# Kernel optimization log

Measured on AMD Instinct MI355X. Metric: run time of the kernel, lower is better.

## Reference

```python
import jax, jax.numpy as jnp
import numpy as np
import math

NUM_EMBED = 1024
EMBED_FEATS = 256
IN_FEATS = 512
COMMITMENT_COST = 0.25
B, T = 16, 4096


def setup_inputs() -> dict:
    key = jax.random.key(0)
    k1, k2, k3, k4 = jax.random.split(key, 4)
    inputs = jax.random.normal(k1, (B, IN_FEATS, T), dtype=jnp.float32)
    # Conv1d(kernel_size=1) == per-position linear: weight [E, C_in], bias [E]
    proj_w = jax.random.normal(k2, (EMBED_FEATS, IN_FEATS), dtype=jnp.float32) / np.sqrt(IN_FEATS)
    proj_b = jax.random.normal(k3, (EMBED_FEATS,), dtype=jnp.float32) * 0.01
    embed = jax.random.normal(k4, (NUM_EMBED, EMBED_FEATS), dtype=jnp.float32)
    return {"inputs": inputs, "proj_w": proj_w, "proj_b": proj_b, "embed": embed}


def reference(inputs, proj_w, proj_b, embed):
    sg = jax.lax.stop_gradient
    b, c_in, t = inputs.shape
    # 1x1 conv projection then transpose(1,-1): [B, T, E]
    x = jnp.einsum('bct,ec->bte', inputs, proj_w) + proj_b
    flat = x.reshape(-1, EMBED_FEATS)  # [B*T, E]
    d2 = (jnp.sum(flat * flat, axis=1, keepdims=True)
          + jnp.sum(embed * embed, axis=1)
          - 2.0 * flat @ embed.T)  # [B*T, num_embed]
    q_idx = jnp.argmin(d2, axis=1)  # [B*T]
    # one-hot @ embed == direct gather (same math, same gradient structure)
    z_q = embed[q_idx].reshape(x.shape)  # [B, T, E]
    vq_loss = jnp.mean((z_q - sg(x)) ** 2)
    commitment_loss = jnp.mean((sg(z_q) - x) ** 2)
    loss = vq_loss + COMMITMENT_COST * commitment_loss
    z_q_st = x + sg(z_q - x)  # straight-through
    n_tokens = flat.shape[0]
    probs = jnp.zeros((NUM_EMBED,), dtype=jnp.float32).at[q_idx].add(1.0) / n_tokens
    log_perplexity = -jnp.sum(probs * jnp.log(probs + 1e-10))
    num_spatial = n_tokens / b
    kldiv_r = math.log(NUM_EMBED) * num_spatial * jnp.ones((b, 1), dtype=jnp.float32)
    z_q_out = jnp.swapaxes(z_q_st, 1, 2)  # [B, E, T]
    return z_q_out, loss, kldiv_r, log_perplexity
```

## Files before the change

### kernel.cpp

```cpp
#include <hip/hip_runtime.h>
#include <hip/hip_bf16.h>
#include <math.h>

#define TT   4096
#define BB   16
#define NTOK 65536
#define CIN  512
#define EF   256
#define NE   1024

typedef __attribute__((ext_vector_type(8))) short bf16x8;
typedef __attribute__((ext_vector_type(4))) float f32x4;

static __device__ __forceinline__ unsigned short f2bf(float f) {
  unsigned int u = __float_as_uint(f);
  u += 0x7fffu + ((u >> 16) & 1u);
  return (unsigned short)(u >> 16);
}

#define GLL(gsrc, ldst) \
  __builtin_amdgcn_global_load_lds((const __attribute__((address_space(1))) void*)(gsrc), \
                                   (__attribute__((address_space(3))) void*)(ldst), 16, 0, 0)

__global__ __launch_bounds__(256) void k_prep(const float* __restrict__ Wf,
                                              const float* __restrict__ Ef,
                                              unsigned short* __restrict__ Wbf,
                                              unsigned short* __restrict__ Ebf,
                                              float* __restrict__ e_norm) {
  int bid = blockIdx.x;
  if (bid < 512) {
    int i = bid * 256 + threadIdx.x;
    Wbf[i] = f2bf(Wf[i]);
  } else if (bid < 1536) {
    int i = (bid - 512) * 256 + threadIdx.x;
    Ebf[i] = f2bf(-2.0f * Ef[i]);
  } else {
    int w = threadIdx.x >> 6, l = threadIdx.x & 63;
    int k = (bid - 1536) * 4 + w;
    const float4 v4 = ((const float4*)(Ef + (size_t)k * EF))[l];
    float s = v4.x * v4.x + v4.y * v4.y + v4.z * v4.z + v4.w * v4.w;
    for (int off = 32; off; off >>= 1) s += __shfl_down(s, off);
    if (l == 0) e_norm[k] = s;
  }
}

__global__ __launch_bounds__(512, 2) void k_fused(const float* __restrict__ in,
                                                  const unsigned short* __restrict__ Wbf,
                                                  const float* __restrict__ bias,
                                                  const unsigned short* __restrict__ Ebf,
                                                  const float* __restrict__ e_norm,
                                                  const float* __restrict__ embed,
                                                  unsigned int* __restrict__ hist,
                                                  float* __restrict__ sse,
                                                  float* __restrict__ out) {
  __shared__ unsigned short lds[36864];
  unsigned short* abuf = lds;
  unsigned short* xs = lds;

  int tid = threadIdx.x;
  int w = tid >> 6, l = tid & 63;
  int l15 = l & 15, quad = l >> 4;
  int tq = w & 1, eq = w >> 1;
  int cg = w & 3, th = w >> 2;
  int tok0 = blockIdx.x * 128;
  const float* src = in + (size_t)(tok0 >> 12) * CIN * TT + (tok0 & 4095);

  f32x4 acc[4][4];
#pragma unroll
  for (int a = 0; a < 4; ++a)
#pragma unroll
    for (int b = 0; b < 4; ++b) acc[a][b] = (f32x4){0.f, 0.f, 0.f, 0.f};

  float v0[16], v1[16];
  {
    const float* sA = src + (size_t)(cg * 16) * TT + th * 64 + l;
#pragma unroll
    for (int i = 0; i < 16; ++i) v0[i] = __builtin_nontemporal_load(&sA[(size_t)i * TT]);
    __builtin_amdgcn_sched_barrier(0);
#pragma unroll
    for (int i = 0; i < 4; ++i) {
      int g = i * 512 + tid;
      int row = g >> 3, pc = g & 7, lc = pc ^ (row & 7);
      GLL(Wbf + (size_t)row * CIN + lc * 8, lds + 4096 + g * 8);
    }
    __builtin_amdgcn_sched_barrier(0);
    const float* sB = src + (size_t)(64 + cg * 16) * TT + th * 64 + l;
#pragma unroll
    for (int i = 0; i < 16; ++i) v1[i] = __builtin_nontemporal_load(&sB[(size_t)i * TT]);
    __builtin_amdgcn_sched_barrier(0);
  }
  int trow = th * 64 + l;
#pragma unroll
  for (int ks = 0; ks < 8; ++ks) {
    unsigned short* wb = lds + 4096 + (ks & 1) * 16384;
    const float* vc = (ks & 1) ? v1 : v0;
#pragma unroll
    for (int cc = 0; cc < 2; ++cc) {
      alignas(16) unsigned short tmp[8];
#pragma unroll
      for (int j = 0; j < 8; ++j) tmp[j] = f2bf(vc[cc * 8 + j]);
      int c8 = cg * 2 + cc;
      int pc2 = c8 ^ (trow & 7);
      *(bf16x8*)(abuf + trow * 64 + pc2 * 8) = *(const bf16x8*)tmp;
    }
    if (ks < 7) {
#pragma unroll
      for (int i = 0; i < 4; ++i) {
        int g = i * 512 + tid;
        int row = g >> 3, pc = g & 7, lc = pc ^ (row & 7);
        GLL(Wbf + (size_t)row * CIN + (ks + 1) * 64 + lc * 8,
            lds + 4096 + ((ks + 1) & 1) * 16384 + g * 8);
      }
    }
    __builtin_amdgcn_sched_barrier(0);
    if (ks < 6) {
      float* vn = (ks & 1) ? v1 : v0;
      const float* sN = src + (size_t)((ks + 2) * 64 + cg * 16) * TT + th * 64 + l;
#pragma unroll
      for (int i = 0; i < 16; ++i) vn[i] = __builtin_nontemporal_load(&sN[(size_t)i * TT]);
    }
    __builtin_amdgcn_sched_barrier(0);
    if (ks < 6)       asm volatile("s_waitcnt vmcnt(36) lgkmcnt(0)\n\ts_barrier" ::: "memory");
    else if (ks == 6) asm volatile("s_waitcnt vmcnt(20) lgkmcnt(0)\n\ts_barrier" ::: "memory");
    else              asm volatile("s_waitcnt vmcnt(0) lgkmcnt(0)\n\ts_barrier" ::: "memory");
#pragma unroll
    for (int kstep = 0; kstep < 2; ++kstep) {
      int ck = kstep * 4 + quad;
      bf16x8 af4[4], bfr[4];
#pragma unroll
      for (int msub = 0; msub < 4; ++msub) {
        int row = tq * 64 + msub * 16 + l15;
        int pa = ck ^ (row & 7);
        af4[msub] = *(const bf16x8*)(abuf + row * 64 + pa * 8);
      }
#pragma unroll
      for (int nsub = 0; nsub < 4; ++nsub) {
        int row = eq * 64 + nsub * 16 + l15;
        int pb = ck ^ (row & 7);
        bfr[nsub] = *(const bf16x8*)(wb + row * 64 + pb * 8);
      }
      __builtin_amdgcn_s_setprio(1);
#pragma unroll
      for (int msub = 0; msub < 4; ++msub)
#pragma unroll
        for (int nsub = 0; nsub < 4; ++nsub)
          acc[msub][nsub] = __builtin_amdgcn_mfma_f32_16x16x32_bf16(af4[msub], bfr[nsub],
                                                                    acc[msub][nsub], 0, 0, 0);
      __builtin_amdgcn_s_setprio(0);
    }
    asm volatile("s_waitcnt lgkmcnt(0)\n\ts_barrier" ::: "memory");
  }

  float xsq = 0.f;
#pragma unroll
  for (int nsub = 0; nsub < 4; ++nsub) {
    int e = eq * 64 + nsub * 16 + l15;
    float bv = bias[e];
    int cx = e >> 3;
#pragma unroll
    for (int msub = 0; msub < 4; ++msub)
#pragma unroll
      for (int reg = 0; reg < 4; ++reg) {
        int m = tq * 64 + msub * 16 + quad * 4 + reg;
        float x = acc[msub][nsub][reg] + bv;
        xsq += x * x;
        int pcx = cx ^ (m & 31);
        xs[m * 256 + pcx * 8 + (e & 7)] = f2bf(x);
      }
  }
  __syncthreads();

  int g3 = w & 3, h = w >> 2;
  bf16x8 af[2][8];
#pragma unroll
  for (int msub = 0; msub < 2; ++msub)
#pragma unroll
    for (int kst = 0; kst < 8; ++kst) {
      int row = g3 * 32 + msub * 16 + l15;
      int c32 = kst * 4 + quad;
      int pcx = c32 ^ (row & 31);
      af[msub][kst] = *(const bf16x8*)(xs + row * 256 + pcx * 8);
    }
  __syncthreads();

  float* entab = (float*)(lds + 32768);
  {
    float2 ev = *(const float2*)(e_norm + (tid << 1));
    *(float2*)(entab + (tid << 1)) = ev;
  }
  __builtin_amdgcn_sched_barrier(0);
#pragma unroll
  for (int c = 0; c < 3; ++c)
#pragma unroll
    for (int i = 0; i < 2; ++i) {
      int g = i * 512 + tid;
      int row = g >> 5, pcc = g & 31, lc = pcc ^ row;
      GLL(Ebf + (size_t)(c * 32 + row) * EF + lc * 8, lds + c * 8192 + g * 8);
    }
  __builtin_amdgcn_sched_barrier(0);

  float best_v[2][4];
  int best_i[2][4];
#pragma unroll
  for (int a = 0; a < 2; ++a)
#pragma unroll
    for (int b = 0; b < 4; ++b) { best_v[a][b] = 3.0e38f; best_i[a][b] = 0; }

  int r3 = h * 16 + l15;
#pragma unroll 1
  for (int chunk = 0; chunk < 32; ++chunk) {
    unsigned short* eb = lds + (chunk & 3) * 8192;
    int c0 = chunk * 32;
    if (chunk < 29) {
      unsigned short* ebn = lds + ((chunk + 3) & 3) * 8192;
#pragma unroll
      for (int i = 0; i < 2; ++i) {
        int g = i * 512 + tid;
        int row = g >> 5, pcc = g & 31, lc = pcc ^ row;
        GLL(Ebf + (size_t)(c0 + 96 + row) * EF + lc * 8, ebn + g * 8);
      }
      __builtin_amdgcn_sched_barrier(0);
      asm volatile("s_waitcnt vmcnt(6) lgkmcnt(0)\n\ts_barrier" ::: "memory");
    } else {
      asm volatile("s_waitcnt vmcnt(0) lgkmcnt(0)\n\ts_barrier" ::: "memory");
    }
    float en = entab[c0 + r3];
    f32x4 dacc[2];
    dacc[0] = (f32x4){en, en, en, en};
    dacc[1] = dacc[0];
    __builtin_amdgcn_s_setprio(1);
#pragma unroll
    for (int kst = 0; kst < 8; ++kst) {
      int cc = kst * 4 + quad;
      int pc = cc ^ r3;
      bf16x8 bfr = *(const bf16x8*)(eb + r3 * 256 + pc * 8);
      dacc[0] = __builtin_amdgcn_mfma_f32_16x16x32_bf16(af[0][kst], bfr, dacc[0], 0, 0, 0);
      dacc[1] = __builtin_amdgcn_mfma_f32_16x16x32_bf16(af[1][kst], bfr, dacc[1], 0, 0, 0);
    }
    __builtin_amdgcn_s_setprio(0);
    int code = c0 + r3;
#pragma unroll
    for (int msub = 0; msub < 2; ++msub)
#pragma unroll
      for (int reg = 0; reg < 4; ++reg) {
        float vv = dacc[msub][reg];
        if (vv < best_v[msub][reg]) { best_v[msub][reg] = vv; best_i[msub][reg] = code; }
      }
    asm volatile("s_waitcnt lgkmcnt(0)\n\ts_barrier" ::: "memory");
  }

#pragma unroll
  for (int msub = 0; msub < 2; ++msub)
#pragma unroll
    for (int reg = 0; reg < 4; ++reg) {
      float vv = best_v[msub][reg];
      int idx = best_i[msub][reg];
#pragma unroll
      for (int off = 8; off; off >>= 1) {
        float ov = __shfl_xor(vv, off, 16);
        int oi = __shfl_xor(idx, off, 16);
        if (ov < vv || (ov == vv && oi < idx)) { vv = ov; idx = oi; }
      }
      best_v[msub][reg] = vv;
      best_i[msub][reg] = idx;
    }
  float* red_v = (float*)lds;
  int* red_i = (int*)lds + 256;
  float* xred = (float*)lds + 512;
  float* svred = (float*)lds + 520;
  int* fidx_w = (int*)lds + 544;
  if (l15 == 0) {
#pragma unroll
    for (int msub = 0; msub < 2; ++msub)
#pragma unroll
      for (int reg = 0; reg < 4; ++reg) {
        int tokloc = g3 * 32 + msub * 16 + quad * 4 + reg;
        red_v[h * 128 + tokloc] = best_v[msub][reg];
        red_i[h * 128 + tokloc] = best_i[msub][reg];
      }
  }
  for (int off = 32; off; off >>= 1) xsq += __shfl_down(xsq, off);
  if (l == 0) xred[w] = xsq;
  __syncthreads();
  if (tid < 128) {
    float v0r = red_v[tid], v1r = red_v[128 + tid];
    int i0 = red_i[tid], i1 = red_i[128 + tid];
    float vv; int idx;
    if (v1r < v0r || (v1r == v0r && i1 < i0)) { vv = v1r; idx = i1; } else { vv = v0r; idx = i0; }
    fidx_w[tid] = idx;
    atomicAdd(&hist[idx], 1u);
    for (int off = 32; off; off >>= 1) vv += __shfl_down(vv, off);
    if ((tid & 63) == 0) svred[tid >> 6] = vv;
  }
  __syncthreads();
  if (tid == 0) {
    float tot = svred[0] + svred[1];
#pragma unroll
    for (int i = 0; i < 8; ++i) tot += xred[i];
    atomicAdd(sse, tot);
  }

  const int* fidx = (const int*)lds + 544;
  float* zq = (float*)lds + 1024;
  int bnum = tok0 >> 12, t0 = tok0 & 4095;
  float* outb = out + (((size_t)bnum * EF) << 12) + t0;
#pragma unroll 1
  for (int et = 0; et < 4; ++et) {
    int e0 = et * 64;
#pragma unroll
    for (int rr = 0; rr < 4; ++rr) {
      int tl = rr * 32 + (tid >> 4);
      const float4 g4 = *(const float4*)(embed + (size_t)fidx[tl] * EF + e0 + (tid & 15) * 4);
      float* zr = zq + tl * 65 + (tid & 15) * 4;
      zr[0] = g4.x; zr[1] = g4.y; zr[2] = g4.z; zr[3] = g4.w;
    }
    __syncthreads();
#pragma unroll
    for (int rr = 0; rr < 4; ++rr) {
      int e = rr * 16 + (tid >> 5);
      float* orow = outb + ((size_t)(e0 + e) << 12);
#pragma unroll
      for (int j = 0; j < 4; ++j) {
        int t = (tid & 31) + 32 * j;
        __builtin_nontemporal_store(zq[t * 65 + e], &orow[t]);
      }
    }
    if (et < 3) __syncthreads();
  }
}

__global__ __launch_bounds__(256) void k_final(const unsigned int* __restrict__ hist,
                                               const float* __restrict__ sse,
                                               float* __restrict__ out) {
  __shared__ float red[4];
  int tid = threadIdx.x;
  float local = 0.f;
  for (int i = tid; i < NE; i += 256) {
    float p = (float)hist[i] * (1.0f / 65536.0f);
    local -= p * logf(p + 1e-10f);
  }
  for (int off = 32; off; off >>= 1) local += __shfl_down(local, off);
  if ((tid & 63) == 0) red[tid >> 6] = local;
  __syncthreads();
  if (tid == 0) {
    float lp = red[0] + red[1] + red[2] + red[3];
    out[16777216] = 1.25f * sse[0] / 16777216.0f;
    out[16777233] = lp;
  }
  if (tid < 16) out[16777217 + tid] = 6.93147180559945f * 4096.0f;
}

extern "C" void kernel_launch(void* const* d_in, const int* in_sizes, int n_in,
                              void* d_out, int out_size, void* d_ws, size_t ws_size,
                              hipStream_t stream) {
  const float* inputs = (const float*)d_in[0];
  const float* proj_w = (const float*)d_in[1];
  const float* proj_b = (const float*)d_in[2];
  const float* embed = (const float*)d_in[3];
  float* out = (float*)d_out;
  char* ws = (char*)d_ws;

  unsigned short* Wbf  = (unsigned short*)(ws);
  unsigned short* Ebf  = (unsigned short*)(ws + 262144);
  float* e_norm        = (float*)(ws + 786432);
  unsigned int* hist   = (unsigned int*)(ws + 1052672);
  float* sse           = (float*)(ws + 1056768);
  if (ws_size < 1056772) return;

  hipMemsetAsync(ws + 1052672, 0, 4100, stream);

  k_prep<<<1792, 256, 0, stream>>>(proj_w, embed, Wbf, Ebf, e_norm);
  k_fused<<<512, 512, 0, stream>>>(inputs, Wbf, proj_b, Ebf, e_norm, embed, hist, sse, out);
  k_final<<<1, 256, 0, stream>>>(hist, sse, out);
}
```

Measured before the change: 293.5 us.

## Fold final reduction into fused kernel and drop per-chunk codebook barrier

Replaces the memset and the separate single-block finalize kernel with zeroing inside the prep kernel and a last-block-done atomic counter in the fused kernel, which computes perplexity and loss in-kernel. This removes two launches. The codebook chunk loop now uses one waitcnt plus barrier per iteration, issued before the next prefetch, instead of two barriers. The weight staging region in LDS is moved to a larger offset so it no longer overlaps the area used for other buffers. The risks are extra LDS use per block, which could lower occupancy, and the added complexity of ordering the atomic completion counter correctly.

```diff
diff --git a/kernel.cpp b/kernel.cpp
--- a/kernel.cpp
+++ b/kernel.cpp
@@ -26,7 +26,10 @@
                                               const float* __restrict__ Ef,
                                               unsigned short* __restrict__ Wbf,
                                               unsigned short* __restrict__ Ebf,
-                                              float* __restrict__ e_norm) {
+                                              float* __restrict__ e_norm,
+                                              unsigned int* __restrict__ hist,
+                                              float* __restrict__ sse,
+                                              unsigned int* __restrict__ cnt) {
   int bid = blockIdx.x;
   if (bid < 512) {
     int i = bid * 256 + threadIdx.x;
@@ -34,13 +37,17 @@
   } else if (bid < 1536) {
     int i = (bid - 512) * 256 + threadIdx.x;
     Ebf[i] = f2bf(-2.0f * Ef[i]);
-  } else {
+  } else if (bid < 1792) {
     int w = threadIdx.x >> 6, l = threadIdx.x & 63;
     int k = (bid - 1536) * 4 + w;
     const float4 v4 = ((const float4*)(Ef + (size_t)k * EF))[l];
     float s = v4.x * v4.x + v4.y * v4.y + v4.z * v4.z + v4.w * v4.w;
     for (int off = 32; off; off >>= 1) s += __shfl_down(s, off);
     if (l == 0) e_norm[k] = s;
+  } else {
+    int tid = threadIdx.x;
+    *(uint4*)(hist + tid * 4) = (uint4){0u, 0u, 0u, 0u};
+    if (tid == 0) { *sse = 0.f; *cnt = 0u; }
   }
 }
 
@@ -52,8 +59,9 @@
                                                   const float* __restrict__ embed,
                                                   unsigned int* __restrict__ hist,
                                                   float* __restrict__ sse,
+                                                  unsigned int* __restrict__ cnt,
                                                   float* __restrict__ out) {
-  __shared__ unsigned short lds[36864];
+  __shared__ unsigned short lds[40960];
   unsigned short* abuf = lds;
   unsigned short* xs = lds;
 
@@ -81,7 +89,7 @@
     for (int i = 0; i < 4; ++i) {
       int g = i * 512 + tid;
       int row = g >> 3, pc = g & 7, lc = pc ^ (row & 7);
-      GLL(Wbf + (size_t)row * CIN + lc * 8, lds + 4096 + g * 8);
+      GLL(Wbf + (size_t)row * CIN + lc * 8, lds + 8192 + g * 8);
     }
     __builtin_amdgcn_sched_barrier(0);
     const float* sB = src + (size_t)(64 + cg * 16) * TT + th * 64 + l;
@@ -92,7 +100,7 @@
   int trow = th * 64 + l;
 #pragma unroll
   for (int ks = 0; ks < 8; ++ks) {
-    unsigned short* wb = lds + 4096 + (ks & 1) * 16384;
+    unsigned short* wb = lds + 8192 + (ks & 1) * 16384;
     const float* vc = (ks & 1) ? v1 : v0;
 #pragma unroll
     for (int cc = 0; cc < 2; ++cc) {
@@ -109,7 +117,7 @@
         int g = i * 512 + tid;
         int row = g >> 3, pc = g & 7, lc = pc ^ (row & 7);
         GLL(Wbf + (size_t)row * CIN + (ks + 1) * 64 + lc * 8,
-            lds + 4096 + ((ks + 1) & 1) * 16384 + g * 8);
+            lds + 8192 + ((ks + 1) & 1) * 16384 + g * 8);
       }
     }
     __builtin_amdgcn_sched_barrier(0);
@@ -211,7 +219,10 @@
   for (int chunk = 0; chunk < 32; ++chunk) {
     unsigned short* eb = lds + (chunk & 3) * 8192;
     int c0 = chunk * 32;
-    if (chunk < 29) {
+    if (chunk < 30)       asm volatile("s_waitcnt vmcnt(4) lgkmcnt(0)\n\ts_barrier" ::: "memory");
+    else if (chunk == 30) asm volatile("s_waitcnt vmcnt(2) lgkmcnt(0)\n\ts_barrier" ::: "memory");
+    else                  asm volatile("s_waitcnt vmcnt(0) lgkmcnt(0)\n\ts_barrier" ::: "memory");
+    if (chunk <= 28) {
       unsigned short* ebn = lds + ((chunk + 3) & 3) * 8192;
 #pragma unroll
       for (int i = 0; i < 2; ++i) {
@@ -219,11 +230,8 @@
         int row = g >> 5, pcc = g & 31, lc = pcc ^ row;
         GLL(Ebf + (size_t)(c0 + 96 + row) * EF + lc * 8, ebn + g * 8);
       }
-      __builtin_amdgcn_sched_barrier(0);
-      asm volatile("s_waitcnt vmcnt(6) lgkmcnt(0)\n\ts_barrier" ::: "memory");
-    } else {
-      asm volatile("s_waitcnt vmcnt(0) lgkmcnt(0)\n\ts_barrier" ::: "memory");
-    }
+    }
+    __builtin_amdgcn_sched_barrier(0);
     float en = entab[c0 + r3];
     f32x4 dacc[2];
     dacc[0] = (f32x4){en, en, en, en};
@@ -246,7 +254,6 @@
         float vv = dacc[msub][reg];
         if (vv < best_v[msub][reg]) { best_v[msub][reg] = vv; best_i[msub][reg] = code; }
       }
-    asm volatile("s_waitcnt lgkmcnt(0)\n\ts_barrier" ::: "memory");
   }
 
 #pragma unroll
@@ -327,27 +334,39 @@
     }
     if (et < 3) __syncthreads();
   }
-}
-
-__global__ __launch_bounds__(256) void k_final(const unsigned int* __restrict__ hist,
-                                               const float* __restrict__ sse,
-                                               float* __restrict__ out) {
-  __shared__ float red[4];
-  int tid = threadIdx.x;
-  float local = 0.f;
-  for (int i = tid; i < NE; i += 256) {
-    float p = (float)hist[i] * (1.0f / 65536.0f);
-    local -= p * logf(p + 1e-10f);
-  }
-  for (int off = 32; off; off >>= 1) local += __shfl_down(local, off);
-  if ((tid & 63) == 0) red[tid >> 6] = local;
-  __syncthreads();
+
+  __syncthreads();
+  int* flag = (int*)lds + 672;
   if (tid == 0) {
-    float lp = red[0] + red[1] + red[2] + red[3];
-    out[16777216] = 1.25f * sse[0] / 16777216.0f;
-    out[16777233] = lp;
-  }
-  if (tid < 16) out[16777217 + tid] = 6.93147180559945f * 4096.0f;
+    __threadfence();
+    unsigned int done = __hip_atomic_fetch_add(cnt, 1u, __ATOMIC_ACQ_REL,
+                                               __HIP_MEMORY_SCOPE_AGENT);
+    *flag = (done == 511u) ? 1 : 0;
+  }
+  __syncthreads();
+  if (*flag) {
+    float local = 0.f;
+#pragma unroll
+    for (int i = 0; i < 2; ++i) {
+      unsigned int hv = __hip_atomic_load(&hist[tid + i * 512], __ATOMIC_RELAXED,
+                                          __HIP_MEMORY_SCOPE_AGENT);
+      float p = (float)hv * (1.0f / 65536.0f);
+      local -= p * logf(p + 1e-10f);
+    }
+    for (int off = 32; off; off >>= 1) local += __shfl_down(local, off);
+    float* ered = (float*)lds + 512;
+    if (l == 0) ered[w] = local;
+    __syncthreads();
+    if (tid == 0) {
+      float lp = 0.f;
+#pragma unroll
+      for (int i = 0; i < 8; ++i) lp += ered[i];
+      float sv = __hip_atomic_load(sse, __ATOMIC_RELAXED, __HIP_MEMORY_SCOPE_AGENT);
+      out[16777216] = 1.25f * sv / 16777216.0f;
+      out[16777233] = lp;
+    }
+    if (tid < 16) out[16777217 + tid] = 6.93147180559945f * 4096.0f;
+  }
 }
 
 extern "C" void kernel_launch(void* const* d_in, const int* in_sizes, int n_in,
@@ -365,11 +384,10 @@
   float* e_norm        = (float*)(ws + 786432);
   unsigned int* hist   = (unsigned int*)(ws + 1052672);
   float* sse           = (float*)(ws + 1056768);
-  if (ws_size < 1056772) return;
-
-  hipMemsetAsync(ws + 1052672, 0, 4100, stream);
-
-  k_prep<<<1792, 256, 0, stream>>>(proj_w, embed, Wbf, Ebf, e_norm);
-  k_fused<<<512, 512, 0, stream>>>(inputs, Wbf, proj_b, Ebf, e_norm, embed, hist, sse, out);
-  k_final<<<1, 256, 0, stream>>>(hist, sse, out);
+  unsigned int* cnt    = (unsigned int*)(ws + 1056772);
+  if (ws_size < 1056776) return;
+
+  k_prep<<<1793, 256, 0, stream>>>(proj_w, embed, Wbf, Ebf, e_norm, hist, sse, cnt);
+  k_fused<<<512, 512, 0, stream>>>(inputs, Wbf, proj_b, Ebf, e_norm, embed,
+                                   hist, sse, cnt, out);
 }
```

Result: slower. 312.5 us (+6.5%).
